# Performance work log

Measured on AMD Instinct MI355X. Metric: run time of the kernel, lower is better.

The kernel has to match this reference:

```python
import jax, jax.numpy as jnp
import numpy as np

# Conv2dfft forward (no spectral compression: preserve_energy=None, index_back=None, out_size=None)
# Implements cross-correlation (DL convolution) via rfft2 / irfft2, matching the torch module's
# padding and output-size logic:
#   out_H = H - HH + 1 + 2*pad ; init_fft = H + 2*pad + max(out_H, HH) - 1

PAD = 1  # padding from init_kwargs


def setup_inputs() -> dict:
    key = jax.random.key(0)
    k1, k2, k3 = jax.random.split(key, 3)
    x = jax.random.normal(k1, (32, 128, 32, 32), dtype=jnp.float32)
    w = jax.random.normal(k2, (128, 128, 3, 3), dtype=jnp.float32) * 0.1
    b = jax.random.normal(k3, (128,), dtype=jnp.float32)
    return {"x": x, "w": w, "b": b}


def reference(x, w, b):
    N, C, H, W = x.shape
    F, _, HH, WW = w.shape
    out_H = H - HH + 1 + 2 * PAD
    out_W = W - WW + 1 + 2 * PAD
    init_fft_H = H + 2 * PAD + max(out_H, HH) - 1  # 65
    init_fft_W = W + 2 * PAD + max(out_W, WW) - 1  # 65

    # pad input: explicit conv padding + zero-pad up to FFT grid
    fft_pad_H = init_fft_H - 2 * PAD - H
    fft_pad_W = init_fft_W - 2 * PAD - W
    px = jnp.pad(x, ((0, 0), (0, 0), (PAD, PAD + fft_pad_H), (PAD, PAD + fft_pad_W)))
    pw = jnp.pad(w, ((0, 0), (0, 0), (0, init_fft_H - HH), (0, init_fft_W - WW)))

    xfft = jnp.fft.rfft2(px)                     # [N,C,65,33] complex64
    yfft = jnp.fft.rfft2(pw)                     # [F,C,65,33] complex64

    # cross-correlation: multiply by conj(filter fft), accumulate over input channels
    prod = jnp.einsum('nchw,fchw->nfhw', xfft, jnp.conj(yfft))
    full = jnp.fft.irfft2(prod, s=(init_fft_H, init_fft_W))  # [N,F,65,65]
    out = full[:, :, :out_H, :out_W] + b[None, :, None, None]
    return out
```

## Files before the change

kernel.cpp:

```cpp
#include <hip/hip_runtime.h>


typedef __attribute__((ext_vector_type(8))) short bf16x8;
typedef __attribute__((ext_vector_type(4))) float f32x4;

#define N_IMG 32
#define C_IN  128
#define F_OUT 128
#define HW    32
#define HPAD  34

__device__ __forceinline__ unsigned short f2bf(float f) {
    union { float f; unsigned u; } v; v.f = f;
    unsigned r = v.u + 0x7fffu + ((v.u >> 16) & 1u);
    return (unsigned short)(r >> 16);
}

__global__ __launch_bounds__(256) void pack_kernel(const float* __restrict__ x,
                                                   const float* __restrict__ w,
                                                   unsigned short* __restrict__ xp,
                                                   unsigned short* __restrict__ wpk) {
    __shared__ unsigned short tile[C_IN * HPAD];
    const int tid = threadIdx.x;
    if (blockIdx.x < N_IMG * HPAD) {
        const int n   = blockIdx.x / HPAD;
        const int hp  = blockIdx.x - n * HPAD;
        const unsigned base_out = (unsigned)(n * HPAD + hp) * (HPAD * C_IN);
        if (hp >= 1 && hp <= 32) {
            const int h = hp - 1;
            #pragma unroll
            for (int i = 0; i < 16; ++i) {
                int idx = tid + i * 256;
                int c = idx >> 5, ww = idx & 31;
                tile[c * HPAD + (ww + 1)] = f2bf(x[((n * C_IN + c) * HW + h) * HW + ww]);
            }
            if (tid < C_IN) { tile[tid * HPAD] = 0; tile[tid * HPAD + 33] = 0; }
            __syncthreads();
            #pragma unroll
            for (int i = 0; i < 17; ++i) {
                int idx = tid + i * 256;
                int wp = idx >> 7, c = idx & 127;
                xp[base_out + (unsigned)idx] = tile[c * HPAD + wp];
            }
        } else {
            #pragma unroll
            for (int i = 0; i < 17; ++i) {
                int idx = tid + i * 256;
                xp[base_out + (unsigned)idx] = 0;
            }
        }
    } else {
        int idx = (blockIdx.x - N_IMG * HPAD) * 256 + tid;
        int c8  = idx & 7;
        int f   = (idx >> 3) & 127;
        int qk  = (idx >> 10) & 3;
        int u   = idx >> 12;
        int cc  = u / 9;
        int tap = u - cc * 9;
        wpk[idx] = f2bf(w[(f * C_IN + cc * 32 + qk * 8 + c8) * 9 + tap]);
    }
}

__global__ __launch_bounds__(256, 1) void conv_gemm_kernel(
    const unsigned short* __restrict__ xp,
    const unsigned short* __restrict__ wpk,
    const float* __restrict__ bias,
    float* __restrict__ out)
{
    __shared__ alignas(16) unsigned short lds_x[208 * C_IN];
    __shared__ alignas(16) unsigned short lds_w[3][3 * 4096];

    const int tid  = threadIdx.x;
    const int lane = tid & 63;
    const int wave = tid >> 6;
    const int qk   = lane >> 4;
    const int l15  = lane & 15;

    const int band = blockIdx.x & 7;
    const int n    = blockIdx.x >> 3;
    const int fh   = wave >> 1;
    const int rp   = wave & 1;
    const int f0   = fh * 64;

    const unsigned short* xbase = xp + (unsigned)((n * HPAD + band * 4) * HPAD) * C_IN;
    #pragma unroll
    for (int i = 0; i < 13; ++i) {
        int p = tid + i * 256;
        int row = p >> 4;  if (row > 203) row = 203;
        int lc = (p ^ row) & 15;
        const unsigned short* src = xbase + row * C_IN + lc * 8;
        __builtin_amdgcn_global_load_lds(
            (const __attribute__((address_space(1))) void*)src,
            (__attribute__((address_space(3))) void*)(&lds_x[p * 8]),
            16, 0, 0);
    }

    #define STAGE_W3(ccv, t0v, bufv) do {                                       \
        const unsigned short* wsrc = wpk + ((ccv) * 9 + (t0v)) * 4096;          \
        _Pragma("unroll")                                                       \
        for (int j_ = 0; j_ < 6; ++j_) {                                        \
            int p_ = tid + j_ * 256;                                            \
            __builtin_amdgcn_global_lds(0);                                     \
        }                                                                       \
    } while (0)
    #undef STAGE_W3
    #define STAGE_W3(ccv, t0v, bufv) do {                                       \
        const unsigned short* wsrc = wpk + ((ccv) * 9 + (t0v)) * 4096;          \
        _Pragma("unroll")                                                       \
        for (int j_ = 0; j_ < 6; ++j_) {                                        \
            int p_ = tid + j_ * 256;                                            \
            __builtin_amdgcn_global_load_lds(                                   \
                (const __attribute__((address_space(1))) void*)(wsrc + p_ * 8), \
                (__attribute__((address_space(3))) void*)(&lds_w[bufv][p_ * 8]),\
                16, 0, 0);                                                      \
        }                                                                       \
    } while (0)

    STAGE_W3(0, 0, 0);
    STAGE_W3(0, 3, 1);

    f32x4 acc[4][4];
    #pragma unroll
    for (int mi = 0; mi < 4; ++mi)
        #pragma unroll
        for (int ni = 0; ni < 4; ++ni)
            acc[mi][ni] = (f32x4){0.f, 0.f, 0.f, 0.f};

    int rrb[4];
    #pragma unroll
    for (int ni = 0; ni < 4; ++ni)
        rrb[ni] = (rp * 2 + (ni >> 1)) * HPAD + (ni & 1) * 16 + l15;

    const int af_base = qk * 1024 + (f0 + l15) * 8;

    asm volatile("s_waitcnt vmcnt(6)" ::: "memory");
    __builtin_amdgcn_s_barrier();
    __builtin_amdgcn_sched_barrier(0);

    #define COMPUTE3(bufv, ccv, T0)                                             \
        _Pragma("unroll")                                                       \
        for (int tl = 0; tl < 3; ++tl) {                                        \
            const int tap = (T0) + tl;                                          \
            const int r = tap / 3, s = tap - 3 * (tap / 3);                     \
            bf16x8 af[4], bf[4];                                                \
            _Pragma("unroll")                                                   \
            for (int mi = 0; mi < 4; ++mi)                                      \
                af[mi] = *(const bf16x8*)&lds_w[bufv][tl * 4096 + af_base + mi * 128]; \
            _Pragma("unroll")                                                   \
            for (int ni = 0; ni < 4; ++ni) {                                    \
                int rr = rrb[ni] + r * HPAD + s;                                \
                int ph = ((ccv) * 4 + qk) ^ (rr & 15);                          \
                bf[ni] = *(const bf16x8*)&lds_x[rr * C_IN + ph * 8];            \
            }                                                                   \
            _Pragma("unroll")                                                   \
            for (int mi = 0; mi < 4; ++mi)                                      \
                _Pragma("unroll")                                               \
                for (int ni = 0; ni < 4; ++ni)                                  \
                    acc[mi][ni] = __builtin_amdgcn_mfma_f32_16x16x32_bf16(      \
                        af[mi], bf[ni], acc[mi][ni], 0, 0, 0);                  \
        }

    #define PHASE_FULL(cc2, t02, b2, bcur, ccv, t0v) do {                       \
        STAGE_W3(cc2, t02, b2);                                                 \
        COMPUTE3(bcur, ccv, t0v);                                               \
        asm volatile("s_waitcnt vmcnt(6)" ::: "memory");                        \
        __builtin_amdgcn_s_barrier();                                           \
        __builtin_amdgcn_sched_barrier(0);                                      \
    } while (0)

    PHASE_FULL(0, 6, 2, 0, 0, 0);
    PHASE_FULL(1, 0, 0, 1, 0, 3);
    PHASE_FULL(1, 3, 1, 2, 0, 6);
    PHASE_FULL(1, 6, 2, 0, 1, 0);
    PHASE_FULL(2, 0, 0, 1, 1, 3);
    PHASE_FULL(2, 3, 1, 2, 1, 6);
    PHASE_FULL(2, 6, 2, 0, 2, 0);
    PHASE_FULL(3, 0, 0, 1, 2, 3);
    PHASE_FULL(3, 3, 1, 2, 2, 6);
    PHASE_FULL(3, 6, 2, 0, 3, 0);
    COMPUTE3(1, 3, 3);
    asm volatile("s_waitcnt vmcnt(0)" ::: "memory");
    __builtin_amdgcn_s_barrier();
    __builtin_amdgcn_sched_barrier(0);
    COMPUTE3(2, 3, 6);

    const int h0 = band * 4 + rp * 2;
    #pragma unroll
    for (int mi = 0; mi < 4; ++mi) {
        const int f_base = f0 + mi * 16 + qk * 4;
        float bv[4];
        #pragma unroll
        for (int r2 = 0; r2 < 4; ++r2) bv[r2] = bias[f_base + r2];
        #pragma unroll
        for (int ni = 0; ni < 4; ++ni) {
            const int h  = h0 + (ni >> 1);
            const int w2 = (ni & 1) * 16 + l15;
            #pragma unroll
            for (int r2 = 0; r2 < 4; ++r2) {
                out[((unsigned)(n * F_OUT + f_base + r2) * HW + h) * HW + w2] =
                    acc[mi][ni][r2] + bv[r2];
            }
        }
    }
    #undef STAGE_W3
    #undef COMPUTE3
    #undef PHASE_FULL
}

extern "C" void kernel_launch(void* const* d_in, const int* in_sizes, int n_in,
                              void* d_out, int out_size, void* d_ws, size_t ws_size,
                              hipStream_t stream) {
    const float* x = (const float*)d_in[0];
    const float* w = (const float*)d_in[1];
    const float* b = (const float*)d_in[2];
    float* out = (float*)d_out;

    unsigned short* xp  = (unsigned short*)d_ws;
    unsigned short* wpk = xp + (size_t)N_IMG * HPAD * HPAD * C_IN;

    pack_kernel<<<N_IMG * HPAD + 576, 256, 0, stream>>>(x, w, xp, wpk);
    conv_gemm_kernel<<<N_IMG * 8, 256, 0, stream>>>(xp, wpk, b, out);
}
```

Baseline: 86.06 us.

## Fuse input bf16 conversion and padding into conv GEMM kernel staging

Stops pre-packing the input into a padded bf16 NHWC workspace in a separate pass. The conv kernel now reads fp32 x directly, converts it to bf16 and writes swizzled rows into LDS, zeroing the halo columns and any out-of-range rows itself. The pack kernel shrinks to weight packing only. This removes a full write and re-read of the packed input, but the staging loads are now synchronous scalar fp32 reads that are strided across channels, replacing async global_load_lds.

After: 83.76 us. 1.03x faster.

```diff
diff --git a/kernel.cpp b/kernel.cpp
--- a/kernel.cpp
+++ b/kernel.cpp
@@ -16,58 +16,25 @@
     return (unsigned short)(r >> 16);
 }
 
-__global__ __launch_bounds__(256) void pack_kernel(const float* __restrict__ x,
-                                                   const float* __restrict__ w,
-                                                   unsigned short* __restrict__ xp,
-                                                   unsigned short* __restrict__ wpk) {
-    __shared__ unsigned short tile[C_IN * HPAD];
-    const int tid = threadIdx.x;
-    if (blockIdx.x < N_IMG * HPAD) {
-        const int n   = blockIdx.x / HPAD;
-        const int hp  = blockIdx.x - n * HPAD;
-        const unsigned base_out = (unsigned)(n * HPAD + hp) * (HPAD * C_IN);
-        if (hp >= 1 && hp <= 32) {
-            const int h = hp - 1;
-            #pragma unroll
-            for (int i = 0; i < 16; ++i) {
-                int idx = tid + i * 256;
-                int c = idx >> 5, ww = idx & 31;
-                tile[c * HPAD + (ww + 1)] = f2bf(x[((n * C_IN + c) * HW + h) * HW + ww]);
-            }
-            if (tid < C_IN) { tile[tid * HPAD] = 0; tile[tid * HPAD + 33] = 0; }
-            __syncthreads();
-            #pragma unroll
-            for (int i = 0; i < 17; ++i) {
-                int idx = tid + i * 256;
-                int wp = idx >> 7, c = idx & 127;
-                xp[base_out + (unsigned)idx] = tile[c * HPAD + wp];
-            }
-        } else {
-            #pragma unroll
-            for (int i = 0; i < 17; ++i) {
-                int idx = tid + i * 256;
-                xp[base_out + (unsigned)idx] = 0;
-            }
-        }
-    } else {
-        int idx = (blockIdx.x - N_IMG * HPAD) * 256 + tid;
-        int c8  = idx & 7;
-        int f   = (idx >> 3) & 127;
-        int qk  = (idx >> 10) & 3;
-        int u   = idx >> 12;
-        int cc  = u / 9;
-        int tap = u - cc * 9;
-        wpk[idx] = f2bf(w[(f * C_IN + cc * 32 + qk * 8 + c8) * 9 + tap]);
-    }
+__global__ __launch_bounds__(256) void pack_w_kernel(const float* __restrict__ w,
+                                                     unsigned short* __restrict__ wpk) {
+    int idx = blockIdx.x * 256 + threadIdx.x;
+    int c8  = idx & 7;
+    int f   = (idx >> 3) & 127;
+    int qk  = (idx >> 10) & 3;
+    int u   = idx >> 12;
+    int cc  = u / 9;
+    int tap = u - cc * 9;
+    wpk[idx] = f2bf(w[(f * C_IN + cc * 32 + qk * 8 + c8) * 9 + tap]);
 }
 
 __global__ __launch_bounds__(256, 1) void conv_gemm_kernel(
-    const unsigned short* __restrict__ xp,
+    const float* __restrict__ x,
     const unsigned short* __restrict__ wpk,
     const float* __restrict__ bias,
     float* __restrict__ out)
 {
-    __shared__ alignas(16) unsigned short lds_x[208 * C_IN];
+    __shared__ alignas(16) unsigned short lds_x[204 * C_IN];
     __shared__ alignas(16) unsigned short lds_w[3][3 * 4096];
 
     const int tid  = threadIdx.x;
@@ -82,28 +49,41 @@
     const int rp   = wave & 1;
     const int f0   = fh * 64;
 
-    const unsigned short* xbase = xp + (unsigned)((n * HPAD + band * 4) * HPAD) * C_IN;
-    #pragma unroll
-    for (int i = 0; i < 13; ++i) {
-        int p = tid + i * 256;
-        int row = p >> 4;  if (row > 203) row = 203;
-        int lc = (p ^ row) & 15;
-        const unsigned short* src = xbase + row * C_IN + lc * 8;
-        __builtin_amdgcn_global_load_lds(
-            (const __attribute__((address_space(1))) void*)src,
-            (__attribute__((address_space(3))) void*)(&lds_x[p * 8]),
-            16, 0, 0);
+    if (tid < 192) {
+        int dh = tid / 32, rem = tid & 31;
+        int wp = (rem & 1) * 33, qc = rem >> 1;
+        int rr = dh * 34 + wp;
+        *(bf16x8*)&lds_x[rr * C_IN + ((qc ^ (rr & 15)) << 3)] =
+            (bf16x8){0, 0, 0, 0, 0, 0, 0, 0};
     }
-
-    #define STAGE_W3(ccv, t0v, bufv) do {                                       \
-        const unsigned short* wsrc = wpk + ((ccv) * 9 + (t0v)) * 4096;          \
-        _Pragma("unroll")                                                       \
-        for (int j_ = 0; j_ < 6; ++j_) {                                        \
-            int p_ = tid + j_ * 256;                                            \
-            __builtin_amdgcn_global_lds(0);                                     \
-        }                                                                       \
-    } while (0)
-    #undef STAGE_W3
+    {
+        const int w_    = lane & 31;
+        const int chalf = lane >> 5;
+        for (int dh = 0; dh < 6; ++dh) {
+            const int h = band * 4 - 1 + dh;
+            const bool valid = (h >= 0) && (h < HW);
+            #pragma unroll
+            for (int g2 = 0; g2 < 2; ++g2) {
+                const int c0 = (wave * 2 + g2) * 16 + chalf * 8;
+                bf16x8 v;
+                if (valid) {
+                    #pragma unroll
+                    for (int k = 0; k < 8; ++k) {
+                        float f = x[((n * C_IN + (c0 + k)) * HW + h) * HW + w_];
+                        v[k] = (short)f2bf(f);
+                    }
+                } else {
+                    #pragma unroll
+                    for (int k = 0; k < 8; ++k) v[k] = 0;
+                }
+                const int rr = dh * 34 + (w_ + 1);
+                const int qc = c0 >> 3;
+                *(bf16x8*)&lds_x[rr * C_IN + ((qc ^ (rr & 15)) << 3)] = v;
+            }
+        }
+    }
+    __builtin_amdgcn_sched_barrier(0);
+
     #define STAGE_W3(ccv, t0v, bufv) do {                                       \
         const unsigned short* wsrc = wpk + ((ccv) * 9 + (t0v)) * 4096;          \
         _Pragma("unroll")                                                       \
@@ -118,6 +98,7 @@
 
     STAGE_W3(0, 0, 0);
     STAGE_W3(0, 3, 1);
+    __builtin_amdgcn_sched_barrier(0);
 
     f32x4 acc[4][4];
     #pragma unroll
@@ -133,7 +114,7 @@
 
     const int af_base = qk * 1024 + (f0 + l15) * 8;
 
-    asm volatile("s_waitcnt vmcnt(6)" ::: "memory");
+    asm volatile("s_waitcnt vmcnt(6) lgkmcnt(0)" ::: "memory");
     __builtin_amdgcn_s_barrier();
     __builtin_amdgcn_sched_barrier(0);
 
@@ -215,9 +196,8 @@
     const float* b = (const float*)d_in[2];
     float* out = (float*)d_out;
 
-    unsigned short* xp  = (unsigned short*)d_ws;
-    unsigned short* wpk = xp + (size_t)N_IMG * HPAD * HPAD * C_IN;
-
-    pack_kernel<<<N_IMG * HPAD + 576, 256, 0, stream>>>(x, w, xp, wpk);
-    conv_gemm_kernel<<<N_IMG * 8, 256, 0, stream>>>(xp, wpk, b, out);
-}
+    unsigned short* wpk = (unsigned short*)d_ws;
+
+    pack_w_kernel<<<576, 256, 0, stream>>>(w, wpk);
+    conv_gemm_kernel<<<N_IMG * 8, 256, 0, stream>>>(x, wpk, b, out);
+}
```
